# Kernel optimization log

Hardware: AMD Instinct MI355X
Metric: run time of the kernel (lower is better)

The kernel has to match this reference:

```python
import jax, jax.numpy as jnp
import numpy as np

B, S, D_MODEL, H = 2, 2048, 1024, 16
HD = D_MODEL // H  # 64


def rotate_half(x):
    # pairs (x_even, x_odd) -> (-x_odd, x_even), interleaved back
    x1 = x[..., ::2]
    x2 = x[..., 1::2]
    return jnp.stack([-x2, x1], axis=-1).reshape(x.shape)


def rope_sin_cos(seq_len, head_dim):
    pos = jnp.arange(seq_len, dtype=jnp.float32)
    dim = jnp.arange(head_dim, dtype=jnp.float32)
    theta = 10000.0 ** (-2.0 * jnp.floor(dim / 2.0) / head_dim)
    angles = pos[:, None] * theta[None, :]  # [S, HD]
    return jnp.sin(angles), jnp.cos(angles)


def setup_inputs():
    key = jax.random.key(0)
    ks = jax.random.split(key, 6)
    w_scale = 1.0 / np.sqrt(D_MODEL)
    x = jax.random.normal(ks[0], (B, S, D_MODEL), jnp.float32)
    # causal mask: 1.0 where attention is disallowed (j > i)
    mask = (1.0 - jnp.tril(jnp.ones((S, S), jnp.float32)))[None, None, :, :]
    wq = jax.random.normal(ks[1], (D_MODEL, D_MODEL), jnp.float32) * w_scale
    wk = jax.random.normal(ks[2], (D_MODEL, D_MODEL), jnp.float32) * w_scale
    wv = jax.random.normal(ks[3], (D_MODEL, D_MODEL), jnp.float32) * w_scale
    wo = jax.random.normal(ks[4], (D_MODEL, D_MODEL), jnp.float32) * w_scale
    zeros = jnp.zeros((D_MODEL,), jnp.float32)
    return dict(x=x, mask=mask, wq=wq, bq=zeros, wk=wk, bk=zeros,
                wv=wv, bv=zeros, wo=wo, bo=zeros)


def reference(x, mask, wq, bq, wk, bk, wv, bv, wo, bo):
    b, s, _ = x.shape

    def split_heads(t):  # [B,S,D] -> [B,H,S,HD]
        return t.reshape(b, s, H, HD).transpose(0, 2, 1, 3)

    q = split_heads(x @ wq + bq)
    k = split_heads(x @ wk + bk)
    v = split_heads(x @ wv + bv)

    sin, cos = rope_sin_cos(s, HD)
    sin = sin[None, None, :, :]
    cos = cos[None, None, :, :]
    q = q * cos + rotate_half(q) * sin
    k = k * cos + rotate_half(k) * sin

    logits = jnp.einsum('bhqd,bhkd->bhqk', q, k) / jnp.sqrt(jnp.float32(HD))
    logits = logits + mask * (-1e9)
    attn = jax.nn.softmax(logits, axis=-1)
    out = jnp.einsum('bhqk,bhkd->bhqd', attn, v)  # [B,H,S,HD]
    out = out.transpose(0, 2, 1, 3).reshape(b, s, D_MODEL)
    return out @ wo + bo
```

## Files before the change

kernel.cpp:

```cpp
#include <hip/hip_runtime.h>
#include <hip/hip_bf16.h>


#define S_ 2048
#define DM 1024
#define HD 64

typedef __attribute__((ext_vector_type(8))) short short8;
typedef __attribute__((ext_vector_type(4))) float floatx4;

__device__ __forceinline__ unsigned short f2b(float x) {
  union { __hip_bfloat16 h; unsigned short u; } cv;
  cv.h = __float2bfloat16(x);
  return cv.u;
}

__device__ __forceinline__ unsigned cvt_pk_bf16(float lo, float hi) {
  unsigned r;
  asm("v_cvt_pk_bf16_f32 %0, %1, %2" : "=v"(r) : "v"(lo), "v"(hi));
  return r;
}

__device__ __forceinline__ void gload_lds16(const unsigned short* g, unsigned short* l) {
  typedef const __attribute__((address_space(1))) unsigned int* gp_t;
  typedef __attribute__((address_space(3))) unsigned int* lp_t;
  __builtin_amdgcn_global_load_lds((gp_t)(const void*)g, (lp_t)(void*)l, 16, 0, 0);
}

__global__ void prep_kernel(const float* __restrict__ x,
                            const float* __restrict__ w0, const float* __restrict__ w1,
                            const float* __restrict__ w2, const float* __restrict__ w3,
                            unsigned short* __restrict__ xc,
                            unsigned short* __restrict__ wt,
                            float2* __restrict__ rope) {
  const int bid = blockIdx.x;
  if (bid < 4096) {
    int i = (bid * 256 + threadIdx.x) * 4;
    float4 v = *(const float4*)(x + i);
    ushort4 o;
    o.x = f2b(v.x); o.y = f2b(v.y); o.z = f2b(v.z); o.w = f2b(v.w);
    *(ushort4*)(xc + i) = o;
  } else if (bid < 8192) {
    __shared__ float tile[32][33];
    const int rem = bid - 4096;
    const int z = rem >> 10;
    const int bx = (rem & 1023) & 31;
    const int by = (rem & 1023) >> 5;
    const float* W = (z == 0) ? w0 : (z == 1) ? w1 : (z == 2) ? w2 : w3;
    unsigned short* Wt = wt + (size_t)z * DM * DM;
    const int tx = threadIdx.x & 31;
    const int ty = threadIdx.x >> 5;
    const int k0 = bx * 32;
    const int c0 = by * 32;
#pragma unroll
    for (int i = 0; i < 4; ++i)
      tile[ty + i * 8][tx] = W[(size_t)(k0 + ty + i * 8) * DM + c0 + tx];
    __syncthreads();
#pragma unroll
    for (int i = 0; i < 4; ++i)
      Wt[(size_t)(c0 + ty + i * 8) * DM + k0 + tx] = f2b(tile[tx][ty + i * 8]);
  } else {
    int i = (bid - 8192) * 256 + threadIdx.x;
    int s = i >> 5, d2 = i & 31;
    float th = expf(-(float)d2 * (9.210340371976184f / 32.0f));
    float sn, cs;
    sincosf((float)s * th, &sn, &cs);
    rope[i] = make_float2(cs, sn);
  }
}

__global__ __launch_bounds__(256, 3) void gemm_qkv(
    const unsigned short* __restrict__ A, const unsigned short* __restrict__ Wt,
    const float* __restrict__ bq, const float* __restrict__ bk,
    const float* __restrict__ bv, const float2* __restrict__ rope,
    unsigned short* __restrict__ QKV) {
  __shared__ __attribute__((aligned(16))) unsigned short As[128 * 64];
  __shared__ __attribute__((aligned(16))) unsigned short Bs[128 * 64];
  const int r0 = blockIdx.x * 128;
  const int c0 = blockIdx.y * 128;
  const int t = threadIdx.x;
  const int lane = t & 63;
  const int wv = t >> 6;
  const int wr = (wv >> 1) * 64;
  const int wc = (wv & 1) * 64;
  const int lr = lane & 15;
  const int lg = lane >> 4;

  const int srow = wv * 32 + (lane >> 3);
  const int sseg = ((lane & 7) ^ (lane >> 3)) * 8;
  const unsigned short* Ag = A + (size_t)(r0 + srow) * DM + sseg;
  const unsigned short* Bg = Wt + (size_t)(c0 + srow) * DM + sseg;
  unsigned short* lA = &As[wv * 32 * 64];
  unsigned short* lB = &Bs[wv * 32 * 64];

  floatx4 acc[4][4] = {};
  const int fswz = (lr & 7) << 4;

  for (int k0 = 0; k0 < DM; k0 += 64) {
#pragma unroll
    for (int j = 0; j < 4; ++j) {
      gload_lds16(Ag + k0 + j * 8 * DM, lA + j * 8 * 64);
      gload_lds16(Bg + k0 + j * 8 * DM, lB + j * 8 * 64);
    }
    __syncthreads();
#pragma unroll
    for (int kk = 0; kk < 2; ++kk) {
      short8 af[4], bf[4];
#pragma unroll
      for (int m = 0; m < 4; ++m)
        af[m] = *(const short8*)((char*)As + (wr + m * 16 + lr) * 128 +
                                 ((kk * 64 + lg * 16) ^ fswz));
#pragma unroll
      for (int n = 0; n < 4; ++n)
        bf[n] = *(const short8*)((char*)Bs + (wc + n * 16 + lr) * 128 +
                                 ((kk * 64 + lg * 16) ^ fswz));
#pragma unroll
      for (int m = 0; m < 4; ++m)
#pragma unroll
        for (int n = 0; n < 4; ++n)
          acc[m][n] = __builtin_amdgcn_mfma_f32_16x16x32_bf16(af[m], bf[n], acc[m][n], 0, 0, 0);
    }
    __syncthreads();
  }

  const int mat = blockIdx.y >> 3;
  const float* bias = (mat == 0) ? bq : (mat == 1) ? bk : bv;
  const int rbase = r0 + wr + lg * 4;
  const int cbase = c0 + wc + lr;
#pragma unroll
  for (int n = 0; n < 4; ++n) {
    const int c = cbase + n * 16;
    const int cc = c & (DM - 1);
    const float bvv = bias[cc];
    const int d = c & 63;
    const int h = cc >> 6;
#pragma unroll
    for (int m = 0; m < 4; ++m) {
#pragma unroll
      for (int i = 0; i < 4; ++i) {
        const int r = rbase + m * 16 + i;
        const int s = r & (S_ - 1);
        const int b = r >> 11;
        float v = acc[m][n][i] + bvv;
        float pv = __shfl_xor(v, 1);
        if (mat < 2) {
          float2 cssn = rope[s * 32 + (d >> 1)];
          v = (d & 1) ? fmaf(v, cssn.x, pv * cssn.y) : fmaf(v, cssn.x, -pv * cssn.y);
          if (mat == 0) v *= 0.18033688011112042f;
        }
        QKV[((size_t)((mat << 5) | (b << 4) | h) * S_ + s) * HD + d] = f2b(v);
      }
    }
  }
}

__global__ __launch_bounds__(256, 4) void gemm_out(
    const unsigned short* __restrict__ A, const unsigned short* __restrict__ Wt,
    const float* __restrict__ bias, float* __restrict__ out) {
  __shared__ __attribute__((aligned(16))) unsigned short As[128 * 64];
  __shared__ __attribute__((aligned(16))) unsigned short Bs[64 * 64];
  const int r0 = blockIdx.x * 128;
  const int c0 = blockIdx.y * 64;
  const int t = threadIdx.x;
  const int lane = t & 63;
  const int wv = t >> 6;
  const int wr = (wv >> 1) * 64;
  const int wc = (wv & 1) * 32;
  const int lr = lane & 15;
  const int lg = lane >> 4;

  const int chunk = lane >> 3;
  const int sseg = ((lane & 7) ^ chunk) * 8;
  const unsigned short* Ag = A + (size_t)(r0 + wv * 32 + chunk) * DM + sseg;
  const unsigned short* Bg = Wt + (size_t)(c0 + wv * 16 + chunk) * DM + sseg;
  unsigned short* lA = &As[wv * 32 * 64];
  unsigned short* lB = &Bs[wv * 16 * 64];

  floatx4 acc[4][2] = {};
  const int fswz = (lr & 7) << 4;

  for (int k0 = 0; k0 < DM; k0 += 64) {
#pragma unroll
    for (int j = 0; j < 4; ++j)
      gload_lds16(Ag + k0 + j * 8 * DM, lA + j * 8 * 64);
#pragma unroll
    for (int j = 0; j < 2; ++j)
      gload_lds16(Bg + k0 + j * 8 * DM, lB + j * 8 * 64);
    __syncthreads();
#pragma unroll
    for (int kk = 0; kk < 2; ++kk) {
      short8 af[4], bf[2];
#pragma unroll
      for (int m = 0; m < 4; ++m)
        af[m] = *(const short8*)((char*)As + (wr + m * 16 + lr) * 128 +
                                 ((kk * 64 + lg * 16) ^ fswz));
#pragma unroll
      for (int n = 0; n < 2; ++n)
        bf[n] = *(const short8*)((char*)Bs + (wc + n * 16 + lr) * 128 +
                                 ((kk * 64 + lg * 16) ^ fswz));
#pragma unroll
      for (int m = 0; m < 4; ++m)
#pragma unroll
        for (int n = 0; n < 2; ++n)
          acc[m][n] = __builtin_amdgcn_mfma_f32_16x16x32_bf16(af[m], bf[n], acc[m][n], 0, 0, 0);
    }
    __syncthreads();
  }

  const int rbase = r0 + wr + lg * 4;
  const int cbase = c0 + wc + lr;
#pragma unroll
  for (int n = 0; n < 2; ++n) {
    const int c = cbase + n * 16;
    const float bvv = bias[c];
#pragma unroll
    for (int m = 0; m < 4; ++m) {
#pragma unroll
      for (int i = 0; i < 4; ++i) {
        const int r = rbase + m * 16 + i;
        out[(size_t)r * DM + c] = acc[m][n][i] + bvv;
      }
    }
  }
}

#define ATTN_STEP(TT, BUF, KLA, KLB)                                           \
  do {                                                                         \
    {                  \
      char* Vb = (char*)Vs[BUF];                                               \
      const unsigned* ua = (const unsigned*)&va;                               \
      const unsigned* ub = (const unsigned*)&vb;                               \
      _Pragma("unroll") for (int j = 0; j < 8; ++j) {                          \
        unsigned pkv = __builtin_amdgcn_perm(                                  \
            ub[j >> 1], ua[j >> 1], (j & 1) ? 0x07060302u : 0x05040100u);      \
        *(unsigned*)(Vb + (oct * 8 + j) * 128 + ((4 * kp) ^ (j << 4))) = pkv;  \
      }                                                                        \
    }                                                                          \
    if ((TT) < qt) {                                \
      va = *(const short8*)(Vpref);                                            \
      vb = *(const short8*)(Vpref + 64);                                       \
      Vpref += 4096;                                                           \
    }                                                                          \
                        \
    asm volatile("s_waitcnt lgkmcnt(0)" ::: "memory");                         \
    __builtin_amdgcn_s_barrier();                                              \
                 \
    if ((TT) < qt) asm volatile("s_waitcnt vmcnt(2)" ::: "memory");            \
    else           asm volatile("s_waitcnt vmcnt(0)" ::: "memory");            \
    __builtin_amdgcn_sched_barrier(0);                                         \
    if ((TT) < qt) {                   \
      gload_lds16(Kpref, KLA);                                                 \
      gload_lds16(Kpref + 2048, KLB);                                          \
      Kpref += 4096;                                                           \
    }                                                                          \
                     \
    floatx4 s[4] = {};                                                         \
    __builtin_amdgcn_s_setprio(1);                                             \
    _Pragma("unroll") for (int kk = 0; kk < 2; ++kk) {                         \
      _Pragma("unroll") for (int n = 0; n < 4; ++n) {                          \
        int r = n * 16 + lr;                                                   \
        short8 kf = *(const short8*)((char*)Ks[BUF] + r * 128 +                \
                                     ((kk * 64 + lg * 16) ^ ((r & 7) << 4)));  \
        s[n] = __builtin_amdgcn_mfma_f32_16x16x32_bf16(kf, qf[kk], s[n], 0, 0, 0); \
      }                                                                        \
    }                                                                          \
    __builtin_amdgcn_s_setprio(0);                                             \
    if ((TT) == qt) {                                                          \
      _Pragma("unroll") for (int n = 0; n < 4; ++n)                            \
        _Pragma("unroll") for (int i = 0; i < 4; ++i)                          \
          if (n * 16 + lg * 4 + i > qin) s[n][i] = -1e30f;                     \
    }                                                                          \
                              \
    float ta = fmaxf(fmaxf(s[0][0], s[0][1]), s[0][2]);                        \
    float tb = fmaxf(fmaxf(s[0][3], s[1][0]), s[1][1]);                        \
    float tc = fmaxf(fmaxf(s[1][2], s[1][3]), s[2][0]);                        \
    float td = fmaxf(fmaxf(s[2][1], s[2][2]), s[2][3]);                        \
    float te = fmaxf(fmaxf(s[3][0], s[3][1]), s[3][2]);                        \
    float tm = fmaxf(fmaxf(ta, tb), tc);                                       \
    tm = fmaxf(fmaxf(tm, td), te);                                             \
    tm = fmaxf(tm, s[3][3]);                                                   \
              \
    if (__any(tm > m + 8.f)) {                                                 \
      tm = fmaxf(tm, __shfl_xor(tm, 16));                                      \
      tm = fmaxf(tm, __shfl_xor(tm, 32));                                      \
      const float mn = fmaxf(m, tm);                                           \
      const float al = exp2f(m - mn);                                          \
      m = mn;                                                                  \
      lsum *= al;                                                              \
      _Pragma("unroll") for (int dd = 0; dd < 4; ++dd) o[dd] *= al;            \
    }                                                                          \
    float ps = 0.f;                                                            \
    _Pragma("unroll") for (int n = 0; n < 4; ++n) {                            \
      _Pragma("unroll") for (int i = 0; i < 4; ++i) {                          \
        float p = exp2f(s[n][i] - m);                                          \
        s[n][i] = p;                                                           \
        ps += p;                                                               \
      }                                                                        \
    }                                                                          \
    lsum += ps;                                                                \
                         \
    _Pragma("unroll") for (int n = 0; n < 4; ++n) {                            \
      _Pragma("unroll") for (int hh = 0; hh < 2; ++hh) {                       \
        unsigned pk = cvt_pk_bf16(s[n][2 * hh], s[n][2 * hh + 1]);             \
        *(unsigned*)(Pw + lr * 128 +                                           \
                     (((n * 16 + lg * 4 + 2 * hh) * 2) ^ pswz)) = pk;          \
      }                                                                        \
    }                                                                          \
    short8 pb[2];                                                              \
    _Pragma("unroll") for (int kk = 0; kk < 2; ++kk)                           \
      pb[kk] = *(const short8*)(Pw + lr * 128 + ((kk * 64 + lg * 16) ^ pswz)); \
    __builtin_amdgcn_s_setprio(1);                                             \
    _Pragma("unroll") for (int kk = 0; kk < 2; ++kk)                           \
      _Pragma("unroll") for (int dd = 0; dd < 4; ++dd) {                       \
        int d = dd * 16 + lr;                                                  \
        short8 vbf = *(const short8*)((char*)Vs[BUF] + d * 128 +               \
                                      ((kk * 64 + lg * 16) ^ ((d & 7) << 4))); \
        o[dd] = __builtin_amdgcn_mfma_f32_16x16x32_bf16(vbf, pb[kk], o[dd], 0, 0, 0); \
      }                                                                        \
    __builtin_amdgcn_s_setprio(0);                                             \
  } while (0)

__global__ __launch_bounds__(256, 4) void attn_kernel(
    const unsigned short* __restrict__ Q, const unsigned short* __restrict__ K,
    const unsigned short* __restrict__ V, unsigned short* __restrict__ AttnC) {
  __shared__ __attribute__((aligned(16))) unsigned short Ks[2][64 * 64];
  __shared__ __attribute__((aligned(16))) unsigned short Vs[2][64 * 64];
  __shared__ __attribute__((aligned(16))) unsigned short Ps[4][16 * 64];

  const int bh = blockIdx.x;
  const int qt = 31 - (int)blockIdx.y;
  const int tid = threadIdx.x;
  const int w = tid >> 6;
  const int l = tid & 63;
  const int lg = l >> 4;
  const int lr = l & 15;
  const size_t base = (size_t)bh * S_ * HD;
  const int qin = w * 16 + lr;

  short8 qf[2];
  {
    const unsigned short* Qrow =
        Q + base + (size_t)(qt * 64 + w * 16 + lr) * HD + lg * 8;
    qf[0] = *(const short8*)(Qrow);
    qf[1] = *(const short8*)(Qrow + 32);
  }

  floatx4 o[4] = {};
  float m = -1e30f, lsum = 0.f;

  const int krow = tid >> 3;
  const int kseg = tid & 7;
  const unsigned short* Kpref = K + base + krow * 64 + ((kseg ^ (krow & 7)) * 8);
  unsigned short* const kld0a = &Ks[0][w * 512];
  unsigned short* const kld0b = &Ks[0][2048 + w * 512];
  unsigned short* const kld1a = &Ks[1][w * 512];
  unsigned short* const kld1b = &Ks[1][2048 + w * 512];

  const int oct = tid >> 5;
  const int kp = tid & 31;
  const unsigned short* Vpref = V + base + 2 * kp * 64 + oct * 8;

  short8 va = *(const short8*)(Vpref);
  short8 vb = *(const short8*)(Vpref + 64);
  Vpref += 4096;
  gload_lds16(Kpref, kld0a);
  gload_lds16(Kpref + 2048, kld0b);
  Kpref += 4096;

  char* const Pw = (char*)Ps[w];
  const int pswz = (lr & 7) << 4;

  int t = 0;
#pragma unroll 1
  for (; t + 1 <= qt; t += 2) {
    ATTN_STEP(t, 0, kld1a, kld1b);
    ATTN_STEP(t + 1, 1, kld0a, kld0b);
  }
  if (t <= qt) ATTN_STEP(t, 0, kld1a, kld1b);

  lsum += __shfl_xor(lsum, 16);
  lsum += __shfl_xor(lsum, 32);
  const float inv = 1.f / lsum;
  unsigned short* orow =
      AttnC + (size_t)((bh >> 4) * S_ + qt * 64 + w * 16 + lr) * DM + (bh & 15) * HD;
#pragma unroll
  for (int dd = 0; dd < 4; ++dd) {
    unsigned w0 = cvt_pk_bf16(o[dd][0] * inv, o[dd][1] * inv);
    unsigned w1 = cvt_pk_bf16(o[dd][2] * inv, o[dd][3] * inv);
    *(uint2*)(orow + dd * 16 + lg * 4) = make_uint2(w0, w1);
  }
}

extern "C" void kernel_launch(void* const* d_in, const int* in_sizes, int n_in,
                              void* d_out, int out_size, void* d_ws, size_t ws_size,
                              hipStream_t stream) {
  const float* x = (const float*)d_in[0];
  const float* wq = (const float*)d_in[2];
  const float* bq = (const float*)d_in[3];
  const float* wk = (const float*)d_in[4];
  const float* bk = (const float*)d_in[5];
  const float* wv = (const float*)d_in[6];
  const float* bv = (const float*)d_in[7];
  const float* wo = (const float*)d_in[8];
  const float* bo = (const float*)d_in[9];

  char* ws = (char*)d_ws;
  const size_t MB = 1024ull * 1024ull;
  unsigned short* Xc = (unsigned short*)(ws);
  unsigned short* Wt = (unsigned short*)(ws + 8 * MB);
  unsigned short* QKVb = (unsigned short*)(ws + 16 * MB);
  unsigned short* Ac = (unsigned short*)(ws + 40 * MB);
  float2* rope = (float2*)(ws + 48 * MB);

  prep_kernel<<<8448, 256, 0, stream>>>(x, wq, wk, wv, wo, Xc, Wt, rope);
  gemm_qkv<<<dim3(32, 24), 256, 0, stream>>>(Xc, Wt, bq, bk, bv, rope, QKVb);
  attn_kernel<<<dim3(32, 32), 256, 0, stream>>>(
      QKVb, QKVb + 32ull * S_ * HD, QKVb + 64ull * S_ * HD, Ac);
  gemm_out<<<dim3(32, 16), 256, 0, stream>>>(Ac, Wt + 3ull * DM * DM, bo, (float*)d_out);
}
```

Measured before the change: 109.5 us.

## Fuse x fp32-to-bf16 conversion into QKV GEMM loads; shrink out-proj tiles

Drops the separate pass that converts x to bf16 in the prep kernel. The QKV GEMM now reads fp32 x directly, converts it in registers, and writes it to swizzled LDS, which removes one full read and write of x through global memory. The price is that the A-operand load becomes synchronous register traffic plus extra reads of fp32 data, repeated across 24 column blocks, instead of an async global-to-LDS copy. Separately, the output projection tile shrinks from 128x64 to 64x64, doubling the grid to improve occupancy and wave balance at the cost of less data reuse.

```diff
diff --git a/kernel.cpp b/kernel.cpp
--- a/kernel.cpp
+++ b/kernel.cpp
@@ -27,25 +27,16 @@
   __builtin_amdgcn_global_load_lds((gp_t)(const void*)g, (lp_t)(void*)l, 16, 0, 0);
 }
 
-__global__ void prep_kernel(const float* __restrict__ x,
-                            const float* __restrict__ w0, const float* __restrict__ w1,
+__global__ void prep_kernel(const float* __restrict__ w0, const float* __restrict__ w1,
                             const float* __restrict__ w2, const float* __restrict__ w3,
-                            unsigned short* __restrict__ xc,
                             unsigned short* __restrict__ wt,
                             float2* __restrict__ rope) {
   const int bid = blockIdx.x;
   if (bid < 4096) {
-    int i = (bid * 256 + threadIdx.x) * 4;
-    float4 v = *(const float4*)(x + i);
-    ushort4 o;
-    o.x = f2b(v.x); o.y = f2b(v.y); o.z = f2b(v.z); o.w = f2b(v.w);
-    *(ushort4*)(xc + i) = o;
-  } else if (bid < 8192) {
     __shared__ float tile[32][33];
-    const int rem = bid - 4096;
-    const int z = rem >> 10;
-    const int bx = (rem & 1023) & 31;
-    const int by = (rem & 1023) >> 5;
+    const int z = bid >> 10;
+    const int bx = (bid & 1023) & 31;
+    const int by = (bid & 1023) >> 5;
     const float* W = (z == 0) ? w0 : (z == 1) ? w1 : (z == 2) ? w2 : w3;
     unsigned short* Wt = wt + (size_t)z * DM * DM;
     const int tx = threadIdx.x & 31;
@@ -60,7 +51,7 @@
     for (int i = 0; i < 4; ++i)
       Wt[(size_t)(c0 + ty + i * 8) * DM + k0 + tx] = f2b(tile[tx][ty + i * 8]);
   } else {
-    int i = (bid - 8192) * 256 + threadIdx.x;
+    int i = (bid - 4096) * 256 + threadIdx.x;
     int s = i >> 5, d2 = i & 31;
     float th = expf(-(float)d2 * (9.210340371976184f / 32.0f));
     float sn, cs;
@@ -70,7 +61,7 @@
 }
 
 __global__ __launch_bounds__(256, 3) void gemm_qkv(
-    const unsigned short* __restrict__ A, const unsigned short* __restrict__ Wt,
+    const float* __restrict__ X, const unsigned short* __restrict__ Wt,
     const float* __restrict__ bq, const float* __restrict__ bk,
     const float* __restrict__ bv, const float2* __restrict__ rope,
     unsigned short* __restrict__ QKV) {
@@ -86,11 +77,13 @@
   const int lr = lane & 15;
   const int lg = lane >> 4;
 
-  const int srow = wv * 32 + (lane >> 3);
-  const int sseg = ((lane & 7) ^ (lane >> 3)) * 8;
-  const unsigned short* Ag = A + (size_t)(r0 + srow) * DM + sseg;
-  const unsigned short* Bg = Wt + (size_t)(c0 + srow) * DM + sseg;
-  unsigned short* lA = &As[wv * 32 * 64];
+  const int chunk = lane >> 3;
+  const int s8 = lane & 7;
+  const int gs = s8 ^ chunk;
+  const int arow = wv * 32 + chunk;
+  const float* Xg = X + (size_t)(r0 + arow) * DM + gs * 8;
+  const unsigned short* Bg = Wt + (size_t)(c0 + arow) * DM + gs * 8;
+  unsigned short* lA = &As[arow * 64 + s8 * 8];
   unsigned short* lB = &Bs[wv * 32 * 64];
 
   floatx4 acc[4][4] = {};
@@ -98,9 +91,18 @@
 
   for (int k0 = 0; k0 < DM; k0 += 64) {
 #pragma unroll
+    for (int j = 0; j < 4; ++j)
+      gload_lds16(Bg + k0 + j * 8 * DM, lB + j * 8 * 64);
+#pragma unroll
     for (int j = 0; j < 4; ++j) {
-      gload_lds16(Ag + k0 + j * 8 * DM, lA + j * 8 * 64);
-      gload_lds16(Bg + k0 + j * 8 * DM, lB + j * 8 * 64);
+      float4 p = *(const float4*)(Xg + k0 + j * 8 * DM);
+      float4 q = *(const float4*)(Xg + k0 + j * 8 * DM + 4);
+      uint4 dw;
+      dw.x = cvt_pk_bf16(p.x, p.y);
+      dw.y = cvt_pk_bf16(p.z, p.w);
+      dw.z = cvt_pk_bf16(q.x, q.y);
+      dw.w = cvt_pk_bf16(q.z, q.w);
+      *(uint4*)(lA + j * 8 * 64) = dw;
     }
     __syncthreads();
 #pragma unroll
@@ -157,41 +159,40 @@
 __global__ __launch_bounds__(256, 4) void gemm_out(
     const unsigned short* __restrict__ A, const unsigned short* __restrict__ Wt,
     const float* __restrict__ bias, float* __restrict__ out) {
-  __shared__ __attribute__((aligned(16))) unsigned short As[128 * 64];
+  __shared__ __attribute__((aligned(16))) unsigned short As[64 * 64];
   __shared__ __attribute__((aligned(16))) unsigned short Bs[64 * 64];
-  const int r0 = blockIdx.x * 128;
+  const int r0 = blockIdx.x * 64;
   const int c0 = blockIdx.y * 64;
   const int t = threadIdx.x;
   const int lane = t & 63;
   const int wv = t >> 6;
-  const int wr = (wv >> 1) * 64;
+  const int wr = (wv >> 1) * 32;
   const int wc = (wv & 1) * 32;
   const int lr = lane & 15;
   const int lg = lane >> 4;
 
   const int chunk = lane >> 3;
   const int sseg = ((lane & 7) ^ chunk) * 8;
-  const unsigned short* Ag = A + (size_t)(r0 + wv * 32 + chunk) * DM + sseg;
-  const unsigned short* Bg = Wt + (size_t)(c0 + wv * 16 + chunk) * DM + sseg;
-  unsigned short* lA = &As[wv * 32 * 64];
-  unsigned short* lB = &Bs[wv * 16 * 64];
-
-  floatx4 acc[4][2] = {};
+  const unsigned short* Ag = A + (size_t)(r0 + wv * 8 + chunk) * DM + sseg;
+  const unsigned short* Bg = Wt + (size_t)(c0 + wv * 8 + chunk) * DM + sseg;
+  unsigned short* lA = &As[wv * 8 * 64];
+  unsigned short* lB = &Bs[wv * 8 * 64];
+
+  floatx4 acc[2][2] = {};
   const int fswz = (lr & 7) << 4;
 
   for (int k0 = 0; k0 < DM; k0 += 64) {
 #pragma unroll
-    for (int j = 0; j < 4; ++j)
-      gload_lds16(Ag + k0 + j * 8 * DM, lA + j * 8 * 64);
-#pragma unroll
-    for (int j = 0; j < 2; ++j)
-      gload_lds16(Bg + k0 + j * 8 * DM, lB + j * 8 * 64);
+    for (int j = 0; j < 2; ++j) {
+      gload_lds16(Ag + k0 + j * 32 * DM, lA + j * 32 * 64);
+      gload_lds16(Bg + k0 + j * 32 * DM, lB + j * 32 * 64);
+    }
     __syncthreads();
 #pragma unroll
     for (int kk = 0; kk < 2; ++kk) {
-      short8 af[4], bf[2];
-#pragma unroll
-      for (int m = 0; m < 4; ++m)
+      short8 af[2], bf[2];
+#pragma unroll
+      for (int m = 0; m < 2; ++m)
         af[m] = *(const short8*)((char*)As + (wr + m * 16 + lr) * 128 +
                                  ((kk * 64 + lg * 16) ^ fswz));
 #pragma unroll
@@ -199,7 +200,7 @@
         bf[n] = *(const short8*)((char*)Bs + (wc + n * 16 + lr) * 128 +
                                  ((kk * 64 + lg * 16) ^ fswz));
 #pragma unroll
-      for (int m = 0; m < 4; ++m)
+      for (int m = 0; m < 2; ++m)
 #pragma unroll
         for (int n = 0; n < 2; ++n)
           acc[m][n] = __builtin_amdgcn_mfma_f32_16x16x32_bf16(af[m], bf[n], acc[m][n], 0, 0, 0);
@@ -214,7 +215,7 @@
     const int c = cbase + n * 16;
     const float bvv = bias[c];
 #pragma unroll
-    for (int m = 0; m < 4; ++m) {
+    for (int m = 0; m < 2; ++m) {
 #pragma unroll
       for (int i = 0; i < 4; ++i) {
         const int r = rbase + m * 16 + i;
@@ -406,15 +407,14 @@
 
   char* ws = (char*)d_ws;
   const size_t MB = 1024ull * 1024ull;
-  unsigned short* Xc = (unsigned short*)(ws);
   unsigned short* Wt = (unsigned short*)(ws + 8 * MB);
   unsigned short* QKVb = (unsigned short*)(ws + 16 * MB);
   unsigned short* Ac = (unsigned short*)(ws + 40 * MB);
   float2* rope = (float2*)(ws + 48 * MB);
 
-  prep_kernel<<<8448, 256, 0, stream>>>(x, wq, wk, wv, wo, Xc, Wt, rope);
-  gemm_qkv<<<dim3(32, 24), 256, 0, stream>>>(Xc, Wt, bq, bk, bv, rope, QKVb);
+  prep_kernel<<<4352, 256, 0, stream>>>(wq, wk, wv, wo, Wt, rope);
+  gemm_qkv<<<dim3(32, 24), 256, 0, stream>>>(x, Wt, bq, bk, bv, rope, QKVb);
   attn_kernel<<<dim3(32, 32), 256, 0, stream>>>(
       QKVb, QKVb + 32ull * S_ * HD, QKVb + 64ull * S_ * HD, Ac);
-  gemm_out<<<dim3(32, 16), 256, 0, stream>>>(Ac, Wt + 3ull * DM * DM, bo, (float*)d_out);
-}
+  gemm_out<<<dim3(64, 16), 256, 0, stream>>>(Ac, Wt + 3ull * DM * DM, bo, (float*)d_out);
+}
```

Result: slower. 112.3 us (+2.5%).
